# Performance work log

Hardware: AMD Instinct MI355X
Metric: run time of the kernel (lower is better)

The kernel has to match this reference:

```python
import jax, jax.numpy as jnp
import numpy as np

B, L, D = 4, 2048, 1024
NUM_HEADS = 1
HEAD_DIM = D // NUM_HEADS  # 1024


def setup_inputs() -> dict:
    key = jax.random.key(0)
    ks = jax.random.split(key, 12)
    s = 1.0 / np.sqrt(D)
    return {
        "query": jax.random.normal(ks[0], (B, L, D), jnp.float32),
        "key": jax.random.normal(ks[1], (B, L, D), jnp.float32),
        "value": jax.random.normal(ks[2], (B, L, D), jnp.float32),
        "mask": jax.random.randint(ks[3], (B, 1, L, L), 0, 2, jnp.int32),
        "Wq": jax.random.uniform(ks[4], (D, D * NUM_HEADS), jnp.float32, -s, s),
        "bq": jnp.zeros((D * NUM_HEADS,), jnp.float32),
        "Wk": jax.random.uniform(ks[5], (D, D * NUM_HEADS), jnp.float32, -s, s),
        "bk": jnp.zeros((D * NUM_HEADS,), jnp.float32),
        "Wv": jax.random.uniform(ks[6], (D, D * NUM_HEADS), jnp.float32, -s, s),
        "bv": jnp.zeros((D * NUM_HEADS,), jnp.float32),
        "Wo": jax.random.uniform(ks[7], (D * NUM_HEADS, D), jnp.float32, -s, s),
        "bo": jnp.zeros((D,), jnp.float32),
    }


def reference(query, key, value, mask, Wq, bq, Wk, bk, Wv, bv, Wo, bo):
    b, lq = query.shape[0], query.shape[1]
    lk = key.shape[1]
    # project and split heads: (B, L, H, Dh) -> (B, H, L, Dh)
    Q = (query @ Wq + bq).reshape(b, lq, NUM_HEADS, HEAD_DIM).transpose(0, 2, 1, 3)
    K = (key @ Wk + bk).reshape(b, lk, NUM_HEADS, HEAD_DIM).transpose(0, 2, 1, 3)
    V = (value @ Wv + bv).reshape(b, lk, NUM_HEADS, HEAD_DIM).transpose(0, 2, 1, 3)
    scale = 1.0 / jnp.sqrt(jnp.float32(HEAD_DIM))
    scores = jnp.einsum("bhqd,bhkd->bhqk", Q, K) * scale  # (B,H,Lq,Lk)
    scores = jnp.where(mask == 0, jnp.float32(-1e20), scores)
    attn = jax.nn.softmax(scores, axis=-1)
    out = jnp.einsum("bhqk,bhkd->bhqd", attn, V)  # (B,H,Lq,Dh)
    out = out.transpose(0, 2, 1, 3).reshape(b, lq, NUM_HEADS * HEAD_DIM)
    return out @ Wo + bo
```

## Files before the change

kernel.cpp:

```cpp
#include <hip/hip_runtime.h>

#define B_ 4
#define L_ 2048
#define D_ 1024
#define M_FLAT (B_*L_)
#define NE_ ((size_t)M_FLAT * D_)
#define WE_ ((size_t)D_ * D_)

typedef unsigned short bf16_t;
typedef __attribute__((ext_vector_type(8))) short bf16x8;
typedef __attribute__((ext_vector_type(4))) float f32x4;

__device__ __forceinline__ bf16_t f2bf(float f) {
  union { float f; unsigned int u; } c; c.f = f;
  unsigned int u = c.u;
  unsigned int r = (u + 0x7fffu + ((u >> 16) & 1u)) >> 16;
  return (bf16_t)r;
}
__device__ __forceinline__ float bf2f(bf16_t h) {
  union { unsigned int u; float f; } c; c.u = ((unsigned int)h) << 16;
  return c.f;
}

__device__ __forceinline__ void gload_lds16(const bf16_t* g, bf16_t* l) {
  __builtin_amdgcn_global_load_lds(
      (const __attribute__((address_space(1))) unsigned int*)g,
      (__attribute__((address_space(3))) unsigned int*)l, 16, 0, 0);
}

#define BARRIER() do { asm volatile("" ::: "memory"); \
                       __builtin_amdgcn_s_barrier();  \
                       asm volatile("" ::: "memory"); } while (0)

__global__ __launch_bounds__(256) void prep_cvt(const float* __restrict__ q,
                                                const float* __restrict__ k,
                                                const float* __restrict__ v,
                                                const float* __restrict__ wv,
                                                bf16_t* __restrict__ xq,
                                                bf16_t* __restrict__ wvb) {
  const float* in; bf16_t* out; size_t li;
  int b = blockIdx.x;
  if (b < 4096)       { in = q;  out = xq;            li = (size_t)b * 256 + threadIdx.x; }
  else if (b < 8192)  { in = k;  out = xq + NE_;      li = (size_t)(b - 4096) * 256 + threadIdx.x; }
  else if (b < 12288) { in = v;  out = xq + 2 * NE_;  li = (size_t)(b - 8192) * 256 + threadIdx.x; }
  else                { in = wv; out = wvb;           li = (size_t)(b - 12288) * 256 + threadIdx.x; }
  const float4* p = (const float4*)in + li * 2;
  float4 a = p[0], bb = p[1];
  union { bf16_t h[8]; uint4 u; } r;
  r.h[0] = f2bf(a.x); r.h[1] = f2bf(a.y); r.h[2] = f2bf(a.z); r.h[3] = f2bf(a.w);
  r.h[4] = f2bf(bb.x); r.h[5] = f2bf(bb.y); r.h[6] = f2bf(bb.z); r.h[7] = f2bf(bb.w);
  ((uint4*)out)[li] = r.u;
}

__global__ __launch_bounds__(256) void transpose_cvt3(const float* __restrict__ Wq,
                                                      const float* __restrict__ Wk,
                                                      const float* __restrict__ Wo,
                                                      bf16_t* __restrict__ outbase) {
  __shared__ float t[32][33];
  int zz = blockIdx.z;
  const float* Wsrc = (zz == 0) ? Wq : (zz == 1) ? Wk : Wo;
  bf16_t* Wt = outbase + (size_t)(zz == 2 ? 3 : zz) * WE_;
  int c0 = blockIdx.x * 32, r0 = blockIdx.y * 32;
  int tx = threadIdx.x, ty = threadIdx.y;
#pragma unroll
  for (int i = 0; i < 4; i++)
    t[ty + i * 8][tx] = Wsrc[(size_t)(r0 + ty + i * 8) * D_ + c0 + tx];
  __syncthreads();
#pragma unroll
  for (int i = 0; i < 4; i++)
    Wt[(size_t)(c0 + ty + i * 8) * D_ + r0 + tx] = f2bf(t[tx][ty + i * 8]);
}

__global__ __launch_bounds__(256) void c2_kernel(const float* __restrict__ bv,
                                                 const float* __restrict__ Wo,
                                                 float* __restrict__ c2) {
  int j = blockIdx.x * 256 + threadIdx.x;
  float s = 0.f;
  for (int k = 0; k < D_; k++) s += bv[k] * Wo[(size_t)k * D_ + j];
  c2[j] = s;
}

__global__ __launch_bounds__(256) void pack_mask(const int* __restrict__ mask,
                                                 unsigned long long* __restrict__ bm) {
  size_t gid = (size_t)blockIdx.x * 256 + threadIdx.x;
  int mi = mask[gid];
  unsigned long long b = __ballot(mi != 0);
  if ((threadIdx.x & 63) == 0) bm[gid >> 6] = b;
}

__global__ __launch_bounds__(256) void reduce_rsum(const float* __restrict__ rsp,
                                                   float* __restrict__ rs) {
  int r = blockIdx.x * 256 + threadIdx.x;
  float s = 0.f;
#pragma unroll
  for (int j = 0; j < 32; j++) s += rsp[(size_t)r * 32 + j];
  rs[r] = fmaxf(s, 1e-30f);
}

#define MODE_PROJ 0
#define MODE_S    1
#define MODE_FIN  2
#define MODE_TR   3

template <int BM, int MODE>
__global__ __launch_bounds__(512, 2)
void g8(const bf16_t* __restrict__ Abase, int lda, long strA,
        const bf16_t* __restrict__ Bbase, int ldb, long strB,
        void* __restrict__ outp, long strO, int ldo,
        const float* __restrict__ x0, const float* __restrict__ x1,
        const float* __restrict__ x2,
        const void* __restrict__ auxp, float* __restrict__ rsp,
        int K) {
  constexpr int WROWS = BM / 2;
  constexpr int QAF   = WROWS / 32;
  constexpr int MFR   = WROWS / 16;
  constexpr int AL    = BM / 128;
  constexpr int BL    = 2;
  constexpr int AHB   = WROWS * 128;
  constexpr int BUFB  = (BM + 256) * 128;
  extern __shared__ __align__(16) char smem[];

  const int tid = threadIdx.x, lane = tid & 63, w = tid >> 6;
  const int wm = w >> 2, wn = w & 3;
  const int fr = lane & 15, fs = lane >> 4;
  const int z = blockIdx.z;

  int gx = gridDim.x, nxy = gx * gridDim.y;
  int lin = blockIdx.y * gx + blockIdx.x;
  if ((nxy & 7) == 0) { int q = nxy >> 3; lin = (lin & 7) * q + (lin >> 3); }
  const int xb = lin % gx;
  const int mbase = (lin / gx) * BM, nbase = xb * 256;

  const bf16_t* A  = Abase + (size_t)z * strA;
  const bf16_t* Bt = Bbase + (size_t)z * strB;

  int offA[2][2], offB[2][2];
#pragma unroll
  for (int h = 0; h < 2; h++)
#pragma unroll
    for (int i = 0; i < 2; i++) {
      int c = i * 512 + tid, row = c >> 3;
      int sg = (c & 7) ^ (row & 7);
      if (i < AL) offA[h][i] = (mbase + h * WROWS + row) * lda + sg * 8;
      offB[h][i] = (nbase + h * 128 + row) * ldb + sg * 8;
    }

  const int swz0 = (fs ^ (fr & 7)) * 16;
  const int swz1 = ((4 + fs) ^ (fr & 7)) * 16;

  bf16x8 af[QAF][2], bfv[2][2][2];
  f32x4 acc[MFR][4] = {};

#define STAGE_A(h, kt, bsel) do {                                             \
    char* hb_ = smem + (bsel) * BUFB + (h) * AHB;                             \
    _Pragma("unroll")                                                         \
    for (int i_ = 0; i_ < AL; ++i_)                                           \
      gload_lds16(A + offA[h][i_] + (kt) * 64,                                \
                  (bf16_t*)(hb_ + (i_ * 512 + tid) * 16));                    \
  } while (0)
#define STAGE_B(h, kt, bsel) do {                                             \
    char* hb_ = smem + (bsel) * BUFB + BM * 128 + (h) * 16384;                \
    _Pragma("unroll")                                                         \
    for (int i_ = 0; i_ < BL; ++i_)                                           \
      gload_lds16(Bt + offB[h][i_] + (kt) * 64,                               \
                  (bf16_t*)(hb_ + (i_ * 512 + tid) * 16));                    \
  } while (0)
#define LOAD_A(bsel, mh) do {                                                 \
    const char* ab_ = smem + (bsel) * BUFB + (wm * WROWS) * 128;              \
    _Pragma("unroll")                                                         \
    for (int i_ = 0; i_ < QAF; ++i_) {                                        \
      int rb_ = ((mh) * (WROWS / 2) + i_ * 16 + fr) * 128;                    \
      af[i_][0] = *(const bf16x8*)(ab_ + rb_ + swz0);                         \
      af[i_][1] = *(const bf16x8*)(ab_ + rb_ + swz1);                         \
    }                                                                         \
  } while (0)
#define LOAD_B(bsel, nh) do {                                                 \
    const char* bb_ = smem + (bsel) * BUFB + BM * 128 + (wn * 64) * 128;      \
    _Pragma("unroll")                                                         \
    for (int j_ = 0; j_ < 2; ++j_) {                                          \
      int rb_ = ((nh) * 32 + j_ * 16 + fr) * 128;                             \
      bfv[nh][j_][0] = *(const bf16x8*)(bb_ + rb_ + swz0);                    \
      bfv[nh][j_][1] = *(const bf16x8*)(bb_ + rb_ + swz1);                    \
    }                                                                         \
  } while (0)
#define MFMA_Q(mh, nh) do {                                                   \
    __builtin_amdgcn_s_setprio(1);                                            \
    _Pragma("unroll")                                                         \
    for (int i_ = 0; i_ < QAF; ++i_)                                          \
    _Pragma("unroll")                                                         \
    for (int j_ = 0; j_ < 2; ++j_) {                                          \
      acc[(mh)*QAF + i_][(nh)*2 + j_] = __builtin_amdgcn_mfma_f32_16x16x32_bf16( \
          af[i_][0], bfv[nh][j_][0], acc[(mh)*QAF + i_][(nh)*2 + j_], 0, 0, 0);  \
      acc[(mh)*QAF + i_][(nh)*2 + j_] = __builtin_amdgcn_mfma_f32_16x16x32_bf16( \
          af[i_][1], bfv[nh][j_][1], acc[(mh)*QAF + i_][(nh)*2 + j_], 0, 0, 0);  \
    }                                                                         \
    __builtin_amdgcn_s_setprio(0);                                            \
  } while (0)
#define LGKM0() do { asm volatile("s_waitcnt lgkmcnt(0)" ::: "memory");       \
                     __builtin_amdgcn_sched_barrier(0); } while (0)
#define VMW4() asm volatile("s_waitcnt vmcnt(4)" ::: "memory")

  const int NK = K >> 6, NI = NK >> 1;

  STAGE_B(0, 0, 0); STAGE_B(1, 0, 0); STAGE_A(0, 0, 0); STAGE_A(1, 0, 0);
  STAGE_B(0, 1, 1); STAGE_B(1, 1, 1);
  VMW4(); BARRIER();

  for (int it = 0; it < NI; ++it) {
    const int t1 = 2 * it + 1;
    const int ta = (2 * it + 2 < NK) ? 2 * it + 2 : NK - 1;
    const int tb = (2 * it + 3 < NK) ? 2 * it + 3 : NK - 1;
    LOAD_A(0, 0); LOAD_B(0, 0);
    STAGE_A(0, t1, 1);
    BARRIER(); LGKM0(); MFMA_Q(0, 0); BARRIER();
    LOAD_B(0, 1);
    STAGE_A(1, t1, 1);
    BARRIER(); LGKM0(); MFMA_Q(0, 1); BARRIER();
    LOAD_A(0, 1);
    STAGE_B(0, ta, 0);
    BARRIER(); LGKM0(); MFMA_Q(1, 1); BARRIER();
    STAGE_B(1, ta, 0);
    VMW4();
    BARRIER(); MFMA_Q(1, 0); BARRIER();
    LOAD_A(1, 0); LOAD_B(1, 0);
    STAGE_A(0, ta, 0);
    BARRIER(); LGKM0(); MFMA_Q(0, 0); BARRIER();
    LOAD_B(1, 1);
    STAGE_A(1, ta, 0);
    BARRIER(); LGKM0(); MFMA_Q(0, 1); BARRIER();
    LOAD_A(1, 1);
    STAGE_B(0, tb, 1);
    BARRIER(); LGKM0(); MFMA_Q(1, 1); BARRIER();
    STAGE_B(1, tb, 1);
    VMW4();
    BARRIER(); MFMA_Q(1, 0); BARRIER();
  }
  asm volatile("s_waitcnt vmcnt(0)" ::: "memory");

  const int r0 = mbase + wm * WROWS;
  const int c0 = nbase + wn * 64;

  if constexpr (MODE == MODE_PROJ) {
    BARRIER();
    char* ep = smem + w * AHB;
    if (z < 2) {
      bf16_t* o = (bf16_t*)outp + (size_t)z * strO;
      const float* bias = (z == 0) ? x0 : x1;
      const float scale = (z == 0) ? 0.03125f : 1.0f;
#pragma unroll
      for (int nf = 0; nf < 4; ++nf) {
        float bv = bias[c0 + nf * 16 + fr];
#pragma unroll
        for (int mf = 0; mf < MFR; ++mf)
#pragma unroll
          for (int jj = 0; jj < 4; ++jj) {
            int row = mf * 16 + fs * 4 + jj;
            int slot = (nf * 2 + (fr >> 3)) ^ ((row >> 1) & 7);
            *(bf16_t*)(ep + row * 128 + slot * 16 + (fr & 7) * 2) =
                f2bf((acc[mf][nf][jj] + bv) * scale);
          }
      }
      asm volatile("s_waitcnt lgkmcnt(0)" ::: "memory");
      const int rl = lane >> 3, sl = lane & 7;
#pragma unroll
      for (int i = 0; i < WROWS / 8; ++i) {
        int row = i * 8 + rl;
        int slot = sl ^ ((row >> 1) & 7);
        uint4 vv = *(const uint4*)(ep + row * 128 + slot * 16);
        *(uint4*)&o[(size_t)(r0 + row) * ldo + c0 + sl * 8] = vv;
      }
    } else {
      bf16_t* ob = (bf16_t*)auxp;
      const int bidx = r0 >> 11, rb = r0 & (L_ - 1);
      ob += (size_t)bidx * D_ * L_;
#pragma unroll
      for (int nf = 0; nf < 4; ++nf) {
        int coll = nf * 16 + fr;
        float bv = x2[c0 + coll];
        int xm = (coll & (WROWS / 8 - 1)) << 3;
#pragma unroll
        for (int mf = 0; mf < MFR; ++mf) {
          int rbase = mf * 16 + fs * 4;
          union { bf16_t h[4]; uint2 u; } pk;
#pragma unroll
          for (int jj = 0; jj < 4; ++jj) pk.h[jj] = f2bf(acc[mf][nf][jj] + bv);
          *(uint2*)(ep + coll * (WROWS * 2) + 2 * (rbase ^ xm)) = pk.u;
        }
      }
      asm volatile("s_waitcnt lgkmcnt(0)" ::: "memory");
      constexpr int LPC = WROWS / 8;
      constexpr int CPI = 64 / LPC;
      const int colr = lane / LPC;
      const int rc = (lane % LPC) * 8;
#pragma unroll
      for (int i2 = 0; i2 < LPC; ++i2) {
        int coll = i2 * CPI + colr;
        int xm = (coll & (WROWS / 8 - 1)) << 3;
        uint4 vv = *(const uint4*)(ep + coll * (WROWS * 2) + 2 * (rc ^ xm));
        *(uint4*)&ob[(size_t)(c0 + coll) * L_ + rb + rc] = vv;
      }
    }
  } else if constexpr (MODE == MODE_TR) {
    BARRIER();
    char* ep = smem + w * AHB;
    bf16_t* ob = (bf16_t*)outp;
#pragma unroll
    for (int nf = 0; nf < 4; ++nf) {
      int coll = nf * 16 + fr;
      int xm = (coll & (WROWS / 8 - 1)) << 3;
#pragma unroll
      for (int mf = 0; mf < MFR; ++mf) {
        int rbase = mf * 16 + fs * 4;
        union { bf16_t h[4]; uint2 u; } pk;
#pragma unroll
        for (int jj = 0; jj < 4; ++jj) pk.h[jj] = f2bf(acc[mf][nf][jj]);
        *(uint2*)(ep + coll * (WROWS * 2) + 2 * (rbase ^ xm)) = pk.u;
      }
    }
    asm volatile("s_waitcnt lgkmcnt(0)" ::: "memory");
    constexpr int LPC = WROWS / 8;
    constexpr int CPI = 64 / LPC;
    const int colr = lane / LPC;
    const int rc = (lane % LPC) * 8;
#pragma unroll
    for (int i2 = 0; i2 < LPC; ++i2) {
      int coll = i2 * CPI + colr;
      int xm = (coll & (WROWS / 8 - 1)) << 3;
      uint4 vv = *(const uint4*)(ep + coll * (WROWS * 2) + 2 * (rc ^ xm));
      *(uint4*)&ob[(size_t)(c0 + coll) * ldo + r0 + rc] = vv;
    }
  } else if constexpr (MODE == MODE_S) {
    BARRIER();
    char* ep = smem + w * AHB;
    bf16_t* o = (bf16_t*)outp + (size_t)z * strO;
    const unsigned long long* bw =
        (const unsigned long long*)auxp +
        ((size_t)z * L_ + r0) * 32 + (c0 >> 6);
#pragma unroll
    for (int mf = 0; mf < MFR; ++mf) {
#pragma unroll
      for (int jj = 0; jj < 4; ++jj) {
        int row = mf * 16 + fs * 4 + jj;
        unsigned long long wd = bw[(size_t)row * 32];
        float psum = 0.f;
#pragma unroll
        for (int nf = 0; nf < 4; ++nf) {
          int cbit = nf * 16 + fr;
          float e = ((wd >> cbit) & 1ull) ? __expf(acc[mf][nf][jj]) : 0.0f;
          bf16_t eb = f2bf(e);
          psum += bf2f(eb);
          int slot = (nf * 2 + (fr >> 3)) ^ ((row >> 1) & 7);
          *(bf16_t*)(ep + row * 128 + slot * 16 + (fr & 7) * 2) = eb;
        }
#pragma unroll
        for (int off = 8; off; off >>= 1) psum += __shfl_xor(psum, off, 16);
        if (fr == 0)
          rsp[((size_t)z * L_ + r0 + row) * 32 + xb * 4 + wn] = psum;
      }
    }
    asm volatile("s_waitcnt lgkmcnt(0)" ::: "memory");
    const int rl = lane >> 3, sl = lane & 7;
#pragma unroll
    for (int i = 0; i < WROWS / 8; ++i) {
      int row = i * 8 + rl;
      int slot = sl ^ ((row >> 1) & 7);
      uint4 vv = *(const uint4*)(ep + row * 128 + slot * 16);
      *(uint4*)&o[(size_t)(r0 + row) * ldo + c0 + sl * 8] = vv;
    }
  } else {
    float* o = (float*)outp + (size_t)z * strO;
    const float* rs = x0 + (size_t)z * L_;
#pragma unroll
    for (int mf = 0; mf < MFR; ++mf) {
#pragma unroll
      for (int jj = 0; jj < 4; ++jj) {
        int r = r0 + mf * 16 + fs * 4 + jj;
        float inv = 1.0f / rs[r];
#pragma unroll
        for (int nf = 0; nf < 4; ++nf) {
          int c = c0 + nf * 16 + fr;
          o[(size_t)r * ldo + c] = acc[mf][nf][jj] * inv + x1[c];
        }
      }
    }
  }
#undef STAGE_A
#undef STAGE_B
#undef LOAD_A
#undef LOAD_B
#undef MFMA_Q
#undef LGKM0
#undef VMW4
}

extern "C" void kernel_launch(void* const* d_in, const int* in_sizes, int n_in,
                              void* d_out, int out_size, void* d_ws, size_t ws_size,
                              hipStream_t stream) {
  const float* query = (const float*)d_in[0];
  const float* keyi  = (const float*)d_in[1];
  const float* value = (const float*)d_in[2];
  const int*   mask  = (const int*)d_in[3];
  const float* Wq = (const float*)d_in[4];
  const float* bq = (const float*)d_in[5];
  const float* Wk = (const float*)d_in[6];
  const float* bk = (const float*)d_in[7];
  const float* Wv = (const float*)d_in[8];
  const float* bv = (const float*)d_in[9];
  const float* Wo = (const float*)d_in[10];
  const float* bo = (const float*)d_in[11];

  bf16_t* ws = (bf16_t*)d_ws;
  bf16_t* XQ   = ws;
  bf16_t* XK   = ws + NE_;
  bf16_t* XV   = ws + 2 * NE_;
  bf16_t* WQT  = ws + 3 * NE_;
  bf16_t* WKT  = WQT + WE_;
  bf16_t* W2T  = WKT + WE_;
  bf16_t* WOT  = W2T + WE_;
  bf16_t* WVb  = WOT + WE_;
  bf16_t* Qb   = WVb + WE_;
  bf16_t* Kb   = Qb + NE_;
  bf16_t* VWt  = Kb + NE_;
  float*  rsump= (float*)(VWt + NE_);
  float*  c2p  = rsump + (size_t)B_ * L_;
  float*  rspart = c2p + D_;
  unsigned long long* bmask =
      (unsigned long long*)(rspart + (size_t)B_ * L_ * 32);
  bf16_t* Sb   = ws;

  hipFuncSetAttribute((const void*)g8<256, MODE_PROJ>,
                      hipFuncAttributeMaxDynamicSharedMemorySize, 131072);
  hipFuncSetAttribute((const void*)g8<256, MODE_S>,
                      hipFuncAttributeMaxDynamicSharedMemorySize, 131072);
  hipFuncSetAttribute((const void*)g8<128, MODE_TR>,
                      hipFuncAttributeMaxDynamicSharedMemorySize, 98304);
  hipFuncSetAttribute((const void*)g8<128, MODE_FIN>,
                      hipFuncAttributeMaxDynamicSharedMemorySize, 98304);

  prep_cvt<<<dim3(12800), dim3(256), 0, stream>>>(query, keyi, value, Wv, XQ, WVb);
  pack_mask<<<dim3(65536), dim3(256), 0, stream>>>(mask, bmask);
  transpose_cvt3<<<dim3(32, 32, 3), dim3(32, 8), 0, stream>>>(Wq, Wk, Wo, WQT);
  c2_kernel<<<dim3(4), dim3(256), 0, stream>>>(bv, Wo, c2p);
  g8<128, MODE_TR><<<dim3(4, 8, 1), 512, 98304, stream>>>(
      WVb, D_, 0, WOT, D_, 0, W2T, 0, D_,
      nullptr, nullptr, nullptr, nullptr, nullptr, D_);
  g8<256, MODE_PROJ><<<dim3(4, 32, 3), 512, 131072, stream>>>(
      XQ, D_, (long)NE_, WQT, D_, (long)WE_, Qb, (long)NE_, D_,
      bq, bk, c2p, VWt, nullptr, D_);
  g8<256, MODE_S><<<dim3(8, 8, 4), 512, 131072, stream>>>(
      Qb, D_, (long)L_ * D_, Kb, D_, (long)L_ * D_, Sb, (long)L_ * L_, L_,
      nullptr, nullptr, nullptr, bmask, rspart, D_);
  reduce_rsum<<<dim3(32), dim3(256), 0, stream>>>(rspart, rsump);
  g8<128, MODE_FIN><<<dim3(4, 16, 4), 512, 98304, stream>>>(
      Sb, L_, (long)L_ * L_, VWt, L_, (long)D_ * L_, d_out, (long)L_ * D_, D_,
      rsump, bo, nullptr, nullptr, nullptr, L_);
}
```

Baseline: 262.0 us.

## Restructure GEMM main loop to stage full tiles per half-iteration and shrink projection tile

Rewrites the double-buffered GEMM K-loop so all four A/B sub-tiles of the next K step are staged together between two barriers, instead of staging them in between each MFMA quarter. This removes the per-quarter barrier pairs and lgkmcnt waits, and the vmcnt wait now depends on the A-tile height. It also switches the QKV projection GEMM from 256-row to 128-row tiles, doubling the grid and cutting LDS use. The trade-off is less fine-grained overlap of global loads with compute, and possible LDS read hazards now that barriers and waits between LDS reads and MFMA are gone.

```diff
diff --git a/kernel.cpp b/kernel.cpp
--- a/kernel.cpp
+++ b/kernel.cpp
@@ -196,44 +196,36 @@
     }                                                                         \
     __builtin_amdgcn_s_setprio(0);                                            \
   } while (0)
-#define LGKM0() do { asm volatile("s_waitcnt lgkmcnt(0)" ::: "memory");       \
-                     __builtin_amdgcn_sched_barrier(0); } while (0)
-#define VMW4() asm volatile("s_waitcnt vmcnt(4)" ::: "memory")
+#define VMWN() do {                                                           \
+    if constexpr (AL == 2) asm volatile("s_waitcnt vmcnt(8)" ::: "memory");   \
+    else                   asm volatile("s_waitcnt vmcnt(6)" ::: "memory");   \
+  } while (0)
 
   const int NK = K >> 6, NI = NK >> 1;
 
   STAGE_B(0, 0, 0); STAGE_B(1, 0, 0); STAGE_A(0, 0, 0); STAGE_A(1, 0, 0);
-  STAGE_B(0, 1, 1); STAGE_B(1, 1, 1);
-  VMW4(); BARRIER();
+  STAGE_B(0, 1, 1); STAGE_B(1, 1, 1); STAGE_A(0, 1, 1); STAGE_A(1, 1, 1);
+  VMWN(); BARRIER();
 
   for (int it = 0; it < NI; ++it) {
-    const int t1 = 2 * it + 1;
     const int ta = (2 * it + 2 < NK) ? 2 * it + 2 : NK - 1;
     const int tb = (2 * it + 3 < NK) ? 2 * it + 3 : NK - 1;
-    LOAD_A(0, 0); LOAD_B(0, 0);
-    STAGE_A(0, t1, 1);
-    BARRIER(); LGKM0(); MFMA_Q(0, 0); BARRIER();
-    LOAD_B(0, 1);
-    STAGE_A(1, t1, 1);
-    BARRIER(); LGKM0(); MFMA_Q(0, 1); BARRIER();
-    LOAD_A(0, 1);
-    STAGE_B(0, ta, 0);
-    BARRIER(); LGKM0(); MFMA_Q(1, 1); BARRIER();
-    STAGE_B(1, ta, 0);
-    VMW4();
-    BARRIER(); MFMA_Q(1, 0); BARRIER();
-    LOAD_A(1, 0); LOAD_B(1, 0);
-    STAGE_A(0, ta, 0);
-    BARRIER(); LGKM0(); MFMA_Q(0, 0); BARRIER();
-    LOAD_B(1, 1);
-    STAGE_A(1, ta, 0);
-    BARRIER(); LGKM0(); MFMA_Q(0, 1); BARRIER();
-    LOAD_A(1, 1);
-    STAGE_B(0, tb, 1);
-    BARRIER(); LGKM0(); MFMA_Q(1, 1); BARRIER();
-    STAGE_B(1, tb, 1);
-    VMW4();
-    BARRIER(); MFMA_Q(1, 0); BARRIER();
+    LOAD_A(0, 0); LOAD_B(0, 0); MFMA_Q(0, 0);
+    LOAD_B(0, 1);               MFMA_Q(0, 1);
+    LOAD_A(0, 1);               MFMA_Q(1, 1);
+                                MFMA_Q(1, 0);
+    BARRIER();
+    STAGE_B(0, ta, 0); STAGE_B(1, ta, 0); STAGE_A(0, ta, 0); STAGE_A(1, ta, 0);
+    VMWN();
+    BARRIER();
+    LOAD_A(1, 0); LOAD_B(1, 0); MFMA_Q(0, 0);
+    LOAD_B(1, 1);               MFMA_Q(0, 1);
+    LOAD_A(1, 1);               MFMA_Q(1, 1);
+                                MFMA_Q(1, 0);
+    BARRIER();
+    STAGE_B(0, tb, 1); STAGE_B(1, tb, 1); STAGE_A(0, tb, 1); STAGE_A(1, tb, 1);
+    VMWN();
+    BARRIER();
   }
   asm volatile("s_waitcnt vmcnt(0)" ::: "memory");
 
@@ -389,8 +381,7 @@
 #undef LOAD_A
 #undef LOAD_B
 #undef MFMA_Q
-#undef LGKM0
-#undef VMW4
+#undef VMWN
 }
 
 extern "C" void kernel_launch(void* const* d_in, const int* in_sizes, int n_in,
@@ -428,8 +419,8 @@
       (unsigned long long*)(rspart + (size_t)B_ * L_ * 32);
   bf16_t* Sb   = ws;
 
-  hipFuncSetAttribute((const void*)g8<256, MODE_PROJ>,
-                      hipFuncAttributeMaxDynamicSharedMemorySize, 131072);
+  hipFuncSetAttribute((const void*)g8<128, MODE_PROJ>,
+                      hipFuncAttributeMaxDynamicSharedMemorySize, 98304);
   hipFuncSetAttribute((const void*)g8<256, MODE_S>,
                       hipFuncAttributeMaxDynamicSharedMemorySize, 131072);
   hipFuncSetAttribute((const void*)g8<128, MODE_TR>,
@@ -444,7 +435,7 @@
   g8<128, MODE_TR><<<dim3(4, 8, 1), 512, 98304, stream>>>(
       WVb, D_, 0, WOT, D_, 0, W2T, 0, D_,
       nullptr, nullptr, nullptr, nullptr, nullptr, D_);
-  g8<256, MODE_PROJ><<<dim3(4, 32, 3), 512, 131072, stream>>>(
+  g8<128, MODE_PROJ><<<dim3(4, 64, 3), 512, 98304, stream>>>(
       XQ, D_, (long)NE_, WQT, D_, (long)WE_, Qb, (long)NE_, D_,
       bq, bk, c2p, VWt, nullptr, D_);
   g8<256, MODE_S><<<dim3(8, 8, 4), 512, 131072, stream>>>(
```

Result: no change. 264.2 us (+0.8%).
